# Optimization experiments

Measured on AMD Instinct MI355X. Metric: run time of the kernel, lower is better.

The kernel has to match this reference:

```python
import jax, jax.numpy as jnp
import numpy as np

NL, D, NH, HD, MLP, L = 4, 1280, 16, 80, 5120, 2048
SEG = 512  # patches per packed image


def setup_inputs() -> dict:
    key = jax.random.key(0)
    ks = jax.random.split(key, 16)
    s = 0.02
    # per-segment RoPE frequency table: positions restart at each image boundary
    inv_freq = 1.0 / (10000.0 ** (jnp.arange(0, HD, 2, dtype=jnp.float32) / HD))  # (HD/2,)
    pos = (jnp.arange(L) % SEG).astype(jnp.float32)
    rotary_pos_emb = pos[:, None] * inv_freq[None, :]  # (L, HD/2)
    return {
        "x": jax.random.normal(ks[0], (L, D), jnp.float32),
        "rotary_pos_emb": rotary_pos_emb,
        "cu_seqlens": jnp.array([0, 512, 1024, 1536, 2048], jnp.int32),
        "ln1_g": 1.0 + s * jax.random.normal(ks[1], (NL, D), jnp.float32),
        "ln1_b": s * jax.random.normal(ks[2], (NL, D), jnp.float32),
        "ln2_g": 1.0 + s * jax.random.normal(ks[3], (NL, D), jnp.float32),
        "ln2_b": s * jax.random.normal(ks[4], (NL, D), jnp.float32),
        "qkv_w": s * jax.random.normal(ks[5], (NL, 3 * D, D), jnp.float32),
        "qkv_b": s * jax.random.normal(ks[6], (NL, 3 * D), jnp.float32),
        "proj_w": s * jax.random.normal(ks[7], (NL, D, D), jnp.float32),
        "proj_b": s * jax.random.normal(ks[8], (NL, D), jnp.float32),
        "mlp_w1": s * jax.random.normal(ks[9], (NL, MLP, D), jnp.float32),
        "mlp_b1": s * jax.random.normal(ks[10], (NL, MLP), jnp.float32),
        "mlp_w2": s * jax.random.normal(ks[11], (NL, D, MLP), jnp.float32),
        "mlp_b2": s * jax.random.normal(ks[12], (NL, D), jnp.float32),
    }


def _ln(x, g, b):
    m = jnp.mean(x, axis=-1, keepdims=True)
    v = jnp.mean((x - m) ** 2, axis=-1, keepdims=True)
    return (x - m) * jax.lax.rsqrt(v + 1e-6) * g + b


def _rope(t, cos, sin):
    # t: (L, H, HD); cos/sin: (L, 1, HD)
    half = t.shape[-1] // 2
    rot = jnp.concatenate([-t[..., half:], t[..., :half]], axis=-1)
    return t * cos + rot * sin


def reference(x, rotary_pos_emb, cu_seqlens, ln1_g, ln1_b, ln2_g, ln2_b,
              qkv_w, qkv_b, proj_w, proj_b, mlp_w1, mlp_b1, mlp_w2, mlp_b2):
    Lx = x.shape[0]
    cos = jnp.cos(rotary_pos_emb)
    sin = jnp.sin(rotary_pos_emb)
    cos = jnp.concatenate([cos, cos], axis=-1)[:, None, :]  # (L,1,HD)
    sin = jnp.concatenate([sin, sin], axis=-1)[:, None, :]
    # block-diagonal attention mask from cu_seqlens via segment ids
    seg = jnp.searchsorted(cu_seqlens, jnp.arange(Lx), side="right")  # (L,)
    mask = seg[:, None] == seg[None, :]  # (L,L) bool
    neg = jnp.finfo(jnp.float32).min
    scale = 1.0 / np.sqrt(HD)
    for l in range(qkv_w.shape[0]):
        h = _ln(x, ln1_g[l], ln1_b[l])
        qkv = (h @ qkv_w[l].T + qkv_b[l]).reshape(Lx, 3, NH, HD)
        q, k, v = qkv[:, 0], qkv[:, 1], qkv[:, 2]  # (L,H,HD) each
        q = _rope(q, cos, sin)
        k = _rope(k, cos, sin)
        scores = jnp.einsum("lhd,mhd->hlm", q, k) * scale  # (H,L,L)
        scores = jnp.where(mask[None], scores, neg)
        w = jax.nn.softmax(scores.astype(jnp.float32), axis=-1).astype(x.dtype)
        att = jnp.einsum("hlm,mhd->lhd", w, v).reshape(Lx, NH * HD)
        x = x + att @ proj_w[l].T + proj_b[l]
        h = _ln(x, ln2_g[l], ln2_b[l])
        x = x + jax.nn.gelu(h @ mlp_w1[l].T + mlp_b1[l], approximate=True) @ mlp_w2[l].T + mlp_b2[l]
    return x
```

## Files before the change

kernel.cpp:

```cpp
#include <hip/hip_runtime.h>
#include <cstdint>
#include <cstddef>

typedef unsigned short u16;
typedef __bf16 bf16_t;
typedef bf16_t bf16x8 __attribute__((ext_vector_type(8)));
typedef float f32x4 __attribute__((ext_vector_type(4)));

#define NLAY 4
#define DMODEL 1280
#define NHEAD 16
#define HDIM 80
#define HDP 96
#define MLPD 5120
#define LTOK 2048
#define SEGLEN 512

__device__ __forceinline__ u16 f2bf(float f) {
  union { float f; unsigned u; } x; x.f = f;
  unsigned r = x.u + 0x7fffu + ((x.u >> 16) & 1u);
  return (u16)(r >> 16);
}
__device__ __forceinline__ float bf2f(u16 s) {
  union { unsigned u; float f; } x; x.u = ((unsigned)s) << 16;
  return x.f;
}

#define GLOAD_LDS16(gsrc, ldst) \
  __builtin_amdgcn_global_load_lds((const __attribute__((address_space(1))) void*)(gsrc), \
                                   (__attribute__((address_space(3))) void*)(ldst), 16, 0, 0)

__device__ __forceinline__ void barrier_mem() {
  asm volatile("s_barrier" ::: "memory");
}

#define C0 (3 * DMODEL * DMODEL / 4)
#define C1 (C0 + DMODEL * DMODEL / 4)
#define C2 (C1 + MLPD * DMODEL / 4)
#define C3 (C2 + DMODEL * MLPD / 4)
__global__ __launch_bounds__(256) void cvt4(const float* __restrict__ s_q,
                                            const float* __restrict__ s_p,
                                            const float* __restrict__ s_1,
                                            const float* __restrict__ s_2,
                                            u16* __restrict__ o_q, u16* __restrict__ o_p,
                                            u16* __restrict__ o_1, u16* __restrict__ o_2) {
  int i = blockIdx.x * 256 + threadIdx.x;
  const float* src; u16* dst; int off;
  if (i < C0)      { src = s_q; dst = o_q; off = i; }
  else if (i < C1) { src = s_p; dst = o_p; off = i - C0; }
  else if (i < C2) { src = s_1; dst = o_1; off = i - C1; }
  else if (i < C3) { src = s_2; dst = o_2; off = i - C2; }
  else return;
  const float4 v = reinterpret_cast<const float4*>(src)[off];
  union { u16 s[4]; uint2 u; } o;
  o.s[0] = f2bf(v.x); o.s[1] = f2bf(v.y); o.s[2] = f2bf(v.z); o.s[3] = f2bf(v.w);
  reinterpret_cast<uint2*>(dst)[off] = o.u;
}

__global__ __launch_bounds__(256) void ln_bf16(const float* __restrict__ x,
                                               const float* __restrict__ g,
                                               const float* __restrict__ b,
                                               u16* __restrict__ out) {
  int row = blockIdx.x;
  int t = threadIdx.x;
  const float* xr = x + (size_t)row * DMODEL;
  float v[5]; float s = 0.f, s2 = 0.f;
#pragma unroll
  for (int i = 0; i < 5; i++) { v[i] = xr[t + i * 256]; s += v[i]; s2 += v[i] * v[i]; }
#pragma unroll
  for (int off = 32; off; off >>= 1) { s += __shfl_down(s, off); s2 += __shfl_down(s2, off); }
  __shared__ float ps[4], ps2[4];
  int w = t >> 6;
  if ((t & 63) == 0) { ps[w] = s; ps2[w] = s2; }
  __syncthreads();
  s = ps[0] + ps[1] + ps[2] + ps[3];
  s2 = ps2[0] + ps2[1] + ps2[2] + ps2[3];
  float mean = s * (1.f / DMODEL);
  float var = s2 * (1.f / DMODEL) - mean * mean;
  float inv = rsqrtf(var + 1e-6f);
#pragma unroll
  for (int i = 0; i < 5; i++) {
    int c = t + i * 256;
    out[(size_t)row * DMODEL + c] = f2bf((v[i] - mean) * inv * g[c] + b[c]);
  }
}

template <int EPI>
__global__ __launch_bounds__(512, 4) void gemmhp(const u16* __restrict__ A,
                                                 const u16* __restrict__ B,
                                                 const float* __restrict__ bias,
                                                 u16* __restrict__ Cb,
                                                 int M, int N, int K) {
  __shared__ u16 As[3][128 * 32];
  __shared__ u16 Bs[3][256 * 32];

  int gN = gridDim.x, gM = gridDim.y;
  int flat = blockIdx.x + gN * blockIdx.y;
  int nwg = gN * gM;
  int qc = nwg >> 3, rc = nwg & 7;
  int xcd = flat & 7, pos = flat >> 3;
  int start = (xcd < rc) ? xcd * (qc + 1) : rc * (qc + 1) + (xcd - rc) * qc;
  int swz = start + pos;
  int m0 = (swz % gM) * 128;
  int n0 = (swz / gM) * 256;

  int t = threadIdx.x, lane = t & 63, w = t >> 6;
  int wm = w >> 2, wn = w & 3;
  int r = lane & 15, kq = lane >> 4;
  f32x4 acc[4][4] = {};

  auto stageA = [&](int buf, int k0) {
    int row = t >> 2, s = t & 3;
    int ss = s ^ ((row >> 1) & 3);
    GLOAD_LDS16(A + (size_t)(m0 + row) * K + k0 + ss * 8, &As[buf][t * 8]);
  };
  auto stageB = [&](int buf, int k0) {
#pragma unroll
    for (int i = 0; i < 2; i++) {
      int chunk = i * 512 + t;
      int row = chunk >> 2, s = chunk & 3;
      int ss = s ^ ((row >> 1) & 3);
      GLOAD_LDS16(B + (size_t)(n0 + row) * K + k0 + ss * 8, &Bs[buf][chunk * 8]);
    }
  };

  int NT = K >> 5;
  stageA(0, 0); stageB(0, 0);
  stageA(1, 32); stageB(1, 32);

  int bt = 0;
  for (int kt = 0; kt < NT; kt++) {
    if (kt == NT - 1) asm volatile("s_waitcnt vmcnt(0)" ::: "memory");
    else              asm volatile("s_waitcnt vmcnt(3)" ::: "memory");
    barrier_mem();
    const u16* as = As[bt];
    const u16* bs = Bs[bt];
    int b2 = bt + 2; if (b2 >= 3) b2 -= 3;
    bool st = (kt + 2) < NT;
    int k2 = (kt + 2) << 5;

    bf16x8 af[4], bfv[4];
#pragma unroll
    for (int i = 0; i < 4; i++) {
      int row = wm * 64 + i * 16 + r;
      int ss = kq ^ ((row >> 1) & 3);
      af[i] = *(const bf16x8*)&as[row * 32 + ss * 8];
    }
#pragma unroll
    for (int j = 0; j < 4; j++) {
      int row = wn * 64 + j * 16 + r;
      int ss = kq ^ ((row >> 1) & 3);
      bfv[j] = *(const bf16x8*)&bs[row * 32 + ss * 8];
    }
    if (st) { stageA(b2, k2); stageB(b2, k2); }
    __builtin_amdgcn_s_setprio(1);
#pragma unroll
    for (int i = 0; i < 4; i++)
#pragma unroll
      for (int j = 0; j < 4; j++)
        acc[i][j] = __builtin_amdgcn_mfma_f32_16x16x32_bf16(af[i], bfv[j], acc[i][j], 0, 0, 0);
    __builtin_amdgcn_s_setprio(0);

    bt++; if (bt == 3) bt = 0;
  }

#pragma unroll
  for (int i = 0; i < 4; i++) {
#pragma unroll
    for (int j = 0; j < 4; j++) {
      int col = n0 + wn * 64 + j * 16 + r;
      float bv = bias[col];
#pragma unroll
      for (int reg = 0; reg < 4; reg++) {
        int rowg = m0 + wm * 64 + i * 16 + kq * 4 + reg;
        float val = acc[i][j][reg] + bv;
        if (EPI == 2) {
          float z2 = -1.5957691216057308f * fmaf(0.044715f * val, val * val, val);
          float gg = val / (1.f + __expf(z2));
          Cb[(size_t)rowg * N + col] = f2bf(gg);
        } else {
          Cb[(size_t)rowg * N + col] = f2bf(val);
        }
      }
    }
  }
}

template <int EPI, int BM, int BN>
__global__ __launch_bounds__(256) void gemm_bt(const u16* __restrict__ A,
                                               const u16* __restrict__ B,
                                               const float* __restrict__ bias,
                                               float* __restrict__ Cf,
                                               u16* __restrict__ Cb,
                                               int M, int N, int K) {
  constexpr int MI = BM / 32;
  constexpr int NJ = BN / 32;
  constexpr int ACH = BM * 64 / (256 * 8);
  constexpr int BCH = BN * 64 / (256 * 8);
  __shared__ u16 As[2][BM * 64];
  __shared__ u16 Bs[2][BN * 64];

  int gN = gridDim.x, gM = gridDim.y;
  int flat = blockIdx.x + gN * blockIdx.y;
  int nwg = gN * gM;
  int qc = nwg >> 3, rc = nwg & 7;
  int xcd = flat & 7, pos = flat >> 3;
  int start = (xcd < rc) ? xcd * (qc + 1) : rc * (qc + 1) + (xcd - rc) * qc;
  int swz = start + pos;
  int m0 = (swz % gM) * BM;
  int n0 = (swz / gM) * BN;

  int t = threadIdx.x, lane = t & 63, w = t >> 6;
  int wm = w >> 1, wn = w & 1;
  int r = lane & 15, kq = lane >> 4;
  f32x4 acc[MI][NJ] = {};

  auto stage = [&](int buf, int k0) {
#pragma unroll
    for (int i = 0; i < ACH; i++) {
      int chunk = i * 256 + t;
      int row = chunk >> 3, s = chunk & 7;
      int ss = s ^ (row & 7);
      GLOAD_LDS16(A + (size_t)(m0 + row) * K + k0 + ss * 8, &As[buf][chunk * 8]);
    }
#pragma unroll
    for (int i = 0; i < BCH; i++) {
      int chunk = i * 256 + t;
      int row = chunk >> 3, s = chunk & 7;
      int ss = s ^ (row & 7);
      GLOAD_LDS16(B + (size_t)(n0 + row) * K + k0 + ss * 8, &Bs[buf][chunk * 8]);
    }
  };

  auto compute = [&](int buf) {
#pragma unroll
    for (int kk = 0; kk < 64; kk += 32) {
      int sx8 = (((kk >> 3) + kq) ^ (r & 7)) * 8;
      bf16x8 af[MI], bfr[NJ];
#pragma unroll
      for (int i = 0; i < MI; i++)
        af[i] = *(const bf16x8*)&As[buf][(wm * (BM / 2) + i * 16 + r) * 64 + sx8];
#pragma unroll
      for (int j = 0; j < NJ; j++)
        bfr[j] = *(const bf16x8*)&Bs[buf][(wn * (BN / 2) + j * 16 + r) * 64 + sx8];
#pragma unroll
      for (int i = 0; i < MI; i++)
#pragma unroll
        for (int j = 0; j < NJ; j++)
          acc[i][j] = __builtin_amdgcn_mfma_f32_16x16x32_bf16(af[i], bfr[j], acc[i][j], 0, 0, 0);
    }
  };

  int NT = K >> 6;
  stage(0, 0);
  __syncthreads();
  for (int step = 0; step < NT; step++) {
    int buf = step & 1;
    if (step + 1 < NT) stage(buf ^ 1, (step + 1) * 64);
    compute(buf);
    __syncthreads();
  }

#pragma unroll
  for (int i = 0; i < MI; i++) {
#pragma unroll
    for (int j = 0; j < NJ; j++) {
      int col = n0 + wn * (BN / 2) + j * 16 + r;
      float bv = bias[col];
#pragma unroll
      for (int reg = 0; reg < 4; reg++) {
        int rowg = m0 + wm * (BM / 2) + i * 16 + kq * 4 + reg;
        float val = acc[i][j][reg] + bv;
        if (EPI == 1) {
          Cf[(size_t)rowg * N + col] += val;
        } else {
          Cb[(size_t)rowg * N + col] = f2bf(val);
        }
      }
    }
  }
}

__global__ __launch_bounds__(256) void rope_pack(const u16* __restrict__ qkv,
                                                 const float* __restrict__ rpe,
                                                 u16* __restrict__ qp,
                                                 u16* __restrict__ kp) {
  int l = blockIdx.x;
  int t = threadIdx.x;
  __shared__ float cs[40], sn[40];
  if (t < 40) {
    float a = rpe[l * 40 + t];
    cs[t] = cosf(a);
    sn[t] = sinf(a);
  }
  __syncthreads();
  const u16* row = qkv + (size_t)l * (3 * DMODEL);
  const float scale = 0.11180339887498949f;
#pragma unroll
  for (int i = 0; i < 5; i++) {
    int e = t + i * 256;
    int h = e / HDIM, d = e - h * HDIM;
    int dm = (d < 40) ? d : d - 40;
    float c = cs[dm], s = sn[dm];
    float qv = bf2f(row[h * HDIM + d]);
    float qr = (d < 40) ? -bf2f(row[h * HDIM + d + 40]) : bf2f(row[h * HDIM + d - 40]);
    qp[((size_t)h * LTOK + l) * HDP + d] = f2bf((qv * c + qr * s) * scale);
    float kv = bf2f(row[DMODEL + h * HDIM + d]);
    float kr = (d < 40) ? -bf2f(row[DMODEL + h * HDIM + d + 40]) : bf2f(row[DMODEL + h * HDIM + d - 40]);
    kp[((size_t)h * LTOK + l) * HDP + d] = f2bf(kv * c + kr * s);
  }
  {
    int h = t >> 4, p = t & 15;
    qp[((size_t)h * LTOK + l) * HDP + HDIM + p] = 0;
    kp[((size_t)h * LTOK + l) * HDP + HDIM + p] = 0;
  }
}

__global__ __launch_bounds__(256) void vtrans(const u16* __restrict__ qkv,
                                              u16* __restrict__ vt) {
  int blk = blockIdx.x;
  int h = blk >> 5, lt = blk & 31;
  int t = threadIdx.x;
  __shared__ u16 ld[64][81];
#pragma unroll
  for (int i = 0; i < 20; i++) {
    int idx = t + i * 256;
    int ll = idx / HDIM, d = idx - ll * HDIM;
    ld[ll][d] = qkv[(size_t)(lt * 64 + ll) * (3 * DMODEL) + 2 * DMODEL + h * HDIM + d];
  }
  __syncthreads();
#pragma unroll
  for (int i = 0; i < 20; i++) {
    int idx = t + i * 256;
    int d = idx >> 6, ll = idx & 63;
    vt[((size_t)h * HDIM + d) * LTOK + lt * 64 + ll] = ld[ll][d];
  }
}

__global__ __launch_bounds__(256) void attn(const u16* __restrict__ qp,
                                            const u16* __restrict__ kp,
                                            const u16* __restrict__ vt,
                                            u16* __restrict__ out) {
  int bid = blockIdx.x;
  int h = bid >> 5;
  int seg = (bid >> 3) & 3;
  int qt = bid & 7;
  int t = threadIdx.x, w = t >> 6, lane = t & 63;
  int r = lane & 15, kq = lane >> 4;
  __shared__ u16 P[4][16][512];
  int seg0 = seg * SEGLEN;
  int q0 = seg0 + qt * 64 + w * 16;

  bf16x8 qf[3];
  const u16* qrow = qp + ((size_t)h * LTOK + q0 + r) * HDP;
#pragma unroll
  for (int kk = 0; kk < 3; kk++) qf[kk] = *(const bf16x8*)(qrow + kk * 32 + kq * 8);

  f32x4 sc[32];
#pragma unroll
  for (int j = 0; j < 32; j++) {
    f32x4 a = {0.f, 0.f, 0.f, 0.f};
    const u16* krow = kp + ((size_t)h * LTOK + seg0 + j * 16 + r) * HDP;
#pragma unroll
    for (int kk = 0; kk < 3; kk++) {
      bf16x8 bfr = *(const bf16x8*)(krow + kk * 32 + kq * 8);
      a = __builtin_amdgcn_mfma_f32_16x16x32_bf16(qf[kk], bfr, a, 0, 0, 0);
    }
    sc[j] = a;
  }

#pragma unroll
  for (int rr = 0; rr < 4; rr++) {
    float m = -1e30f;
#pragma unroll
    for (int j = 0; j < 32; j++) m = fmaxf(m, sc[j][rr]);
#pragma unroll
    for (int off = 1; off < 16; off <<= 1) m = fmaxf(m, __shfl_xor(m, off));
    float s = 0.f;
#pragma unroll
    for (int j = 0; j < 32; j++) { float e = __expf(sc[j][rr] - m); sc[j][rr] = e; s += e; }
#pragma unroll
    for (int off = 1; off < 16; off <<= 1) s += __shfl_xor(s, off);
    float inv = 1.f / s;
#pragma unroll
    for (int j = 0; j < 32; j++)
      P[w][kq * 4 + rr][j * 16 + r] = f2bf(sc[j][rr] * inv);
  }
  __syncthreads();

  f32x4 oc[5] = {};
#pragma unroll
  for (int tt = 0; tt < 16; tt++) {
    bf16x8 a = *(const bf16x8*)&P[w][r][tt * 32 + kq * 8];
#pragma unroll
    for (int n = 0; n < 5; n++) {
      const u16* vrow = vt + ((size_t)h * HDIM + n * 16 + r) * LTOK + seg0 + tt * 32 + kq * 8;
      bf16x8 bfr = *(const bf16x8*)vrow;
      oc[n] = __builtin_amdgcn_mfma_f32_16x16x32_bf16(a, bfr, oc[n], 0, 0, 0);
    }
  }
#pragma unroll
  for (int n = 0; n < 5; n++)
#pragma unroll
    for (int reg = 0; reg < 4; reg++) {
      int l = q0 + kq * 4 + reg;
      out[(size_t)l * DMODEL + h * HDIM + n * 16 + r] = f2bf(oc[n][reg]);
    }
}

extern "C" void kernel_launch(void* const* d_in, const int* in_sizes, int n_in,
                              void* d_out, int out_size, void* d_ws, size_t ws_size,
                              hipStream_t stream) {
  (void)in_sizes; (void)n_in; (void)out_size; (void)ws_size;
  const float* x_in   = (const float*)d_in[0];
  const float* rpe    = (const float*)d_in[1];
  const float* ln1_g  = (const float*)d_in[3];
  const float* ln1_b  = (const float*)d_in[4];
  const float* ln2_g  = (const float*)d_in[5];
  const float* ln2_b  = (const float*)d_in[6];
  const float* qkv_w  = (const float*)d_in[7];
  const float* qkv_b  = (const float*)d_in[8];
  const float* proj_w = (const float*)d_in[9];
  const float* proj_b = (const float*)d_in[10];
  const float* mlp_w1 = (const float*)d_in[11];
  const float* mlp_b1 = (const float*)d_in[12];
  const float* mlp_w2 = (const float*)d_in[13];
  const float* mlp_b2 = (const float*)d_in[14];
  float* x = (float*)d_out;

  char* ws = (char*)d_ws;
  size_t off = 0;
  auto alloc = [&](size_t bytes) -> char* {
    char* p = ws + off;
    off = (off + bytes + 255) & ~(size_t)255;
    return p;
  };
  u16* wq  = (u16*)alloc((size_t)3 * DMODEL * DMODEL * 2);
  u16* wp  = (u16*)alloc((size_t)DMODEL * DMODEL * 2);
  u16* w1  = (u16*)alloc((size_t)MLPD * DMODEL * 2);
  u16* w2  = (u16*)alloc((size_t)DMODEL * MLPD * 2);
  u16* hb  = (u16*)alloc((size_t)LTOK * DMODEL * 2);
  u16* qkvb = (u16*)alloc((size_t)LTOK * 3 * DMODEL * 2);
  u16* qp  = (u16*)alloc((size_t)NHEAD * LTOK * HDP * 2);
  u16* kp  = (u16*)alloc((size_t)NHEAD * LTOK * HDP * 2);
  u16* vt  = (u16*)alloc((size_t)NHEAD * HDIM * LTOK * 2);
  u16* att = (u16*)alloc((size_t)LTOK * DMODEL * 2);
  u16* ge  = (u16*)alloc((size_t)LTOK * MLPD * 2);

  hipMemcpyAsync(x, x_in, (size_t)LTOK * DMODEL * sizeof(float),
                 hipMemcpyDeviceToDevice, stream);

  for (int l = 0; l < NLAY; l++) {
    cvt4<<<(C3 + 255) / 256, 256, 0, stream>>>(
        qkv_w + (size_t)l * 3 * DMODEL * DMODEL, proj_w + (size_t)l * DMODEL * DMODEL,
        mlp_w1 + (size_t)l * MLPD * DMODEL, mlp_w2 + (size_t)l * DMODEL * MLPD,
        wq, wp, w1, w2);

    ln_bf16<<<LTOK, 256, 0, stream>>>(x, ln1_g + l * DMODEL, ln1_b + l * DMODEL, hb);
    gemmhp<3><<<dim3(15, 16), 512, 0, stream>>>(
        hb, wq, qkv_b + (size_t)l * 3 * DMODEL, qkvb, LTOK, 3 * DMODEL, DMODEL);
    rope_pack<<<LTOK, 256, 0, stream>>>(qkvb, rpe, qp, kp);
    vtrans<<<NHEAD * 32, 256, 0, stream>>>(qkvb, vt);
    attn<<<NHEAD * 4 * 8, 256, 0, stream>>>(qp, kp, vt, att);
    gemm_bt<1, 64, 64><<<dim3(20, 32), 256, 0, stream>>>(
        att, wp, proj_b + (size_t)l * DMODEL, x, nullptr, LTOK, DMODEL, DMODEL);
    ln_bf16<<<LTOK, 256, 0, stream>>>(x, ln2_g + l * DMODEL, ln2_b + l * DMODEL, hb);
    gemmhp<2><<<dim3(20, 16), 512, 0, stream>>>(
        hb, w1, mlp_b1 + (size_t)l * MLPD, ge, LTOK, MLPD, DMODEL);
    gemm_bt<1, 64, 64><<<dim3(20, 32), 256, 0, stream>>>(
        ge, w2, mlp_b2 + (size_t)l * DMODEL, x, nullptr, LTOK, DMODEL, MLPD);
  }
}
```

Measured before the change: 923.7 us.

## Replace residual GEMMs with 128x128 triple-buffered pipelined kernel

Replaces the 64x64 double-buffered gemm_bt used for the attention projection and MLP down-projection with a new 128x128 tile kernel. It uses BK=32, three LDS buffers with fine-grained vmcnt waits, and raised wave priority around the MFMA block. The goal is more data reuse per tile and better overlap of global loads with compute. The grid shrinks from 640 to 160 workgroups, which may underfill the CUs for the N=1280 GEMMs.

```diff
diff --git a/kernel.cpp b/kernel.cpp
--- a/kernel.cpp
+++ b/kernel.cpp
@@ -186,19 +186,14 @@
   }
 }
 
-template <int EPI, int BM, int BN>
-__global__ __launch_bounds__(256) void gemm_bt(const u16* __restrict__ A,
-                                               const u16* __restrict__ B,
-                                               const float* __restrict__ bias,
-                                               float* __restrict__ Cf,
-                                               u16* __restrict__ Cb,
-                                               int M, int N, int K) {
-  constexpr int MI = BM / 32;
-  constexpr int NJ = BN / 32;
-  constexpr int ACH = BM * 64 / (256 * 8);
-  constexpr int BCH = BN * 64 / (256 * 8);
-  __shared__ u16 As[2][BM * 64];
-  __shared__ u16 Bs[2][BN * 64];
+template <int EPI>
+__global__ __launch_bounds__(256, 3) void gemmdp(const u16* __restrict__ A,
+                                                 const u16* __restrict__ B,
+                                                 const float* __restrict__ bias,
+                                                 float* __restrict__ Cf,
+                                                 int M, int N, int K) {
+  __shared__ u16 As[3][128 * 32];
+  __shared__ u16 Bs[3][128 * 32];
 
   int gN = gridDim.x, gM = gridDim.y;
   int flat = blockIdx.x + gN * blockIdx.y;
@@ -207,75 +202,81 @@
   int xcd = flat & 7, pos = flat >> 3;
   int start = (xcd < rc) ? xcd * (qc + 1) : rc * (qc + 1) + (xcd - rc) * qc;
   int swz = start + pos;
-  int m0 = (swz % gM) * BM;
-  int n0 = (swz / gM) * BN;
+  int m0 = (swz % gM) * 128;
+  int n0 = (swz / gM) * 128;
 
   int t = threadIdx.x, lane = t & 63, w = t >> 6;
   int wm = w >> 1, wn = w & 1;
   int r = lane & 15, kq = lane >> 4;
-  f32x4 acc[MI][NJ] = {};
+  f32x4 acc[4][4] = {};
 
   auto stage = [&](int buf, int k0) {
 #pragma unroll
-    for (int i = 0; i < ACH; i++) {
+    for (int i = 0; i < 2; i++) {
       int chunk = i * 256 + t;
-      int row = chunk >> 3, s = chunk & 7;
-      int ss = s ^ (row & 7);
+      int row = chunk >> 2, s = chunk & 3;
+      int ss = s ^ ((row >> 1) & 3);
       GLOAD_LDS16(A + (size_t)(m0 + row) * K + k0 + ss * 8, &As[buf][chunk * 8]);
     }
 #pragma unroll
-    for (int i = 0; i < BCH; i++) {
+    for (int i = 0; i < 2; i++) {
       int chunk = i * 256 + t;
-      int row = chunk >> 3, s = chunk & 7;
-      int ss = s ^ (row & 7);
+      int row = chunk >> 2, s = chunk & 3;
+      int ss = s ^ ((row >> 1) & 3);
       GLOAD_LDS16(B + (size_t)(n0 + row) * K + k0 + ss * 8, &Bs[buf][chunk * 8]);
     }
   };
 
-  auto compute = [&](int buf) {
-#pragma unroll
-    for (int kk = 0; kk < 64; kk += 32) {
-      int sx8 = (((kk >> 3) + kq) ^ (r & 7)) * 8;
-      bf16x8 af[MI], bfr[NJ];
-#pragma unroll
-      for (int i = 0; i < MI; i++)
-        af[i] = *(const bf16x8*)&As[buf][(wm * (BM / 2) + i * 16 + r) * 64 + sx8];
-#pragma unroll
-      for (int j = 0; j < NJ; j++)
-        bfr[j] = *(const bf16x8*)&Bs[buf][(wn * (BN / 2) + j * 16 + r) * 64 + sx8];
-#pragma unroll
-      for (int i = 0; i < MI; i++)
-#pragma unroll
-        for (int j = 0; j < NJ; j++)
-          acc[i][j] = __builtin_amdgcn_mfma_f32_16x16x32_bf16(af[i], bfr[j], acc[i][j], 0, 0, 0);
-    }
-  };
-
-  int NT = K >> 6;
+  int NT = K >> 5;
   stage(0, 0);
-  __syncthreads();
-  for (int step = 0; step < NT; step++) {
-    int buf = step & 1;
-    if (step + 1 < NT) stage(buf ^ 1, (step + 1) * 64);
-    compute(buf);
-    __syncthreads();
-  }
-
-#pragma unroll
-  for (int i = 0; i < MI; i++) {
-#pragma unroll
-    for (int j = 0; j < NJ; j++) {
-      int col = n0 + wn * (BN / 2) + j * 16 + r;
+  stage(1, 32);
+
+  int bt = 0;
+  for (int kt = 0; kt < NT; kt++) {
+    if (kt == NT - 1) asm volatile("s_waitcnt vmcnt(0)" ::: "memory");
+    else              asm volatile("s_waitcnt vmcnt(4)" ::: "memory");
+    barrier_mem();
+    const u16* as = As[bt];
+    const u16* bs = Bs[bt];
+    int b2 = bt + 2; if (b2 >= 3) b2 -= 3;
+    bool st = (kt + 2) < NT;
+    int k2 = (kt + 2) << 5;
+
+    bf16x8 af[4], bfv[4];
+#pragma unroll
+    for (int i = 0; i < 4; i++) {
+      int row = wm * 64 + i * 16 + r;
+      int ss = kq ^ ((row >> 1) & 3);
+      af[i] = *(const bf16x8*)&as[row * 32 + ss * 8];
+    }
+#pragma unroll
+    for (int j = 0; j < 4; j++) {
+      int row = wn * 64 + j * 16 + r;
+      int ss = kq ^ ((row >> 1) & 3);
+      bfv[j] = *(const bf16x8*)&bs[row * 32 + ss * 8];
+    }
+    if (st) stage(b2, k2);
+    __builtin_amdgcn_s_setprio(1);
+#pragma unroll
+    for (int i = 0; i < 4; i++)
+#pragma unroll
+      for (int j = 0; j < 4; j++)
+        acc[i][j] = __builtin_amdgcn_mfma_f32_16x16x32_bf16(af[i], bfv[j], acc[i][j], 0, 0, 0);
+    __builtin_amdgcn_s_setprio(0);
+
+    bt++; if (bt == 3) bt = 0;
+  }
+
+#pragma unroll
+  for (int i = 0; i < 4; i++) {
+#pragma unroll
+    for (int j = 0; j < 4; j++) {
+      int col = n0 + wn * 64 + j * 16 + r;
       float bv = bias[col];
 #pragma unroll
       for (int reg = 0; reg < 4; reg++) {
-        int rowg = m0 + wm * (BM / 2) + i * 16 + kq * 4 + reg;
-        float val = acc[i][j][reg] + bv;
-        if (EPI == 1) {
-          Cf[(size_t)rowg * N + col] += val;
-        } else {
-          Cb[(size_t)rowg * N + col] = f2bf(val);
-        }
+        int rowg = m0 + wm * 64 + i * 16 + kq * 4 + reg;
+        Cf[(size_t)rowg * N + col] += acc[i][j][reg] + bv;
       }
     }
   }
@@ -462,12 +463,12 @@
     rope_pack<<<LTOK, 256, 0, stream>>>(qkvb, rpe, qp, kp);
     vtrans<<<NHEAD * 32, 256, 0, stream>>>(qkvb, vt);
     attn<<<NHEAD * 4 * 8, 256, 0, stream>>>(qp, kp, vt, att);
-    gemm_bt<1, 64, 64><<<dim3(20, 32), 256, 0, stream>>>(
-        att, wp, proj_b + (size_t)l * DMODEL, x, nullptr, LTOK, DMODEL, DMODEL);
+    gemmdp<1><<<dim3(10, 16), 256, 0, stream>>>(
+        att, wp, proj_b + (size_t)l * DMODEL, x, LTOK, DMODEL, DMODEL);
     ln_bf16<<<LTOK, 256, 0, stream>>>(x, ln2_g + l * DMODEL, ln2_b + l * DMODEL, hb);
     gemmhp<2><<<dim3(20, 16), 512, 0, stream>>>(
         hb, w1, mlp_b1 + (size_t)l * MLPD, ge, LTOK, MLPD, DMODEL);
-    gemm_bt<1, 64, 64><<<dim3(20, 32), 256, 0, stream>>>(
-        ge, w2, mlp_b2 + (size_t)l * DMODEL, x, nullptr, LTOK, DMODEL, MLPD);
-  }
-}
+    gemmdp<1><<<dim3(10, 16), 256, 0, stream>>>(
+        ge, w2, mlp_b2 + (size_t)l * DMODEL, x, LTOK, DMODEL, MLPD);
+  }
+}
```

Measured after the change: 1.078 ms. 16.7% more time.

## Split-K the MLP down-projection with 128x128 tiles and separate reduction

Applied to the files above, without the earlier changes.

Replaces the 64x64-tile down-projection GEMM (K=5120) with a 4-way split-K kernel. It uses 128x128 tiles and a triple-buffered LDS pipeline, and writes fp32 partials into dead workspace buffers starting at hb. A separate reduce kernel then sums the partials, adds the bias and accumulates into the residual x. The aim is more data reuse per tile while keeping enough workgroups to fill the GPU. In exchange, the partials cost extra memory traffic and a second kernel launch per layer.

```diff
diff --git a/kernel.cpp b/kernel.cpp
--- a/kernel.cpp
+++ b/kernel.cpp
@@ -186,6 +186,120 @@
   }
 }
 
+__global__ __launch_bounds__(256, 3) void gemmsk(const u16* __restrict__ A,
+                                                 const u16* __restrict__ B,
+                                                 float* __restrict__ P,
+                                                 int M, int N, int K, int KC) {
+  __shared__ u16 As[3][128 * 32];
+  __shared__ u16 Bs[3][128 * 32];
+
+  int gN = gridDim.x, gM = gridDim.y;
+  int flat = blockIdx.x + gN * blockIdx.y;
+  int nwg = gN * gM;
+  int qc = nwg >> 3, rc = nwg & 7;
+  int xcd = flat & 7, pos = flat >> 3;
+  int start = (xcd < rc) ? xcd * (qc + 1) : rc * (qc + 1) + (xcd - rc) * qc;
+  int swz = start + pos;
+  int m0 = (swz % gM) * 128;
+  int n0 = (swz / gM) * 128;
+  int kbase = blockIdx.z * KC;
+  float* Pz = P + (size_t)blockIdx.z * M * N;
+
+  int t = threadIdx.x, lane = t & 63, w = t >> 6;
+  int wm = w >> 1, wn = w & 1;
+  int r = lane & 15, kq = lane >> 4;
+  f32x4 acc[4][4] = {};
+
+  auto stage = [&](int buf, int k0) {
+#pragma unroll
+    for (int i = 0; i < 2; i++) {
+      int chunk = i * 256 + t;
+      int row = chunk >> 2, s = chunk & 3;
+      int ss = s ^ ((row >> 1) & 3);
+      GLOAD_LDS16(A + (size_t)(m0 + row) * K + k0 + ss * 8, &As[buf][chunk * 8]);
+    }
+#pragma unroll
+    for (int i = 0; i < 2; i++) {
+      int chunk = i * 256 + t;
+      int row = chunk >> 2, s = chunk & 3;
+      int ss = s ^ ((row >> 1) & 3);
+      GLOAD_LDS16(B + (size_t)(n0 + row) * K + k0 + ss * 8, &Bs[buf][chunk * 8]);
+    }
+  };
+
+  int NT = KC >> 5;
+  stage(0, kbase);
+  stage(1, kbase + 32);
+
+  int bt = 0;
+  for (int kt = 0; kt < NT; kt++) {
+    if (kt == NT - 1) asm volatile("s_waitcnt vmcnt(0)" ::: "memory");
+    else              asm volatile("s_waitcnt vmcnt(4)" ::: "memory");
+    barrier_mem();
+    const u16* as = As[bt];
+    const u16* bs = Bs[bt];
+    int b2 = bt + 2; if (b2 >= 3) b2 -= 3;
+    bool st = (kt + 2) < NT;
+    int k2 = kbase + ((kt + 2) << 5);
+
+    bf16x8 af[4], bfv[4];
+#pragma unroll
+    for (int i = 0; i < 4; i++) {
+      int row = wm * 64 + i * 16 + r;
+      int ss = kq ^ ((row >> 1) & 3);
+      af[i] = *(const bf16x8*)&as[row * 32 + ss * 8];
+    }
+#pragma unroll
+    for (int j = 0; j < 4; j++) {
+      int row = wn * 64 + j * 16 + r;
+      int ss = kq ^ ((row >> 1) & 3);
+      bfv[j] = *(const bf16x8*)&bs[row * 32 + ss * 8];
+    }
+    if (st) stage(b2, k2);
+    __builtin_amdgcn_s_setprio(1);
+#pragma unroll
+    for (int i = 0; i < 4; i++)
+#pragma unroll
+      for (int j = 0; j < 4; j++)
+        acc[i][j] = __builtin_amdgcn_mfma_f32_16x16x32_bf16(af[i], bfv[j], acc[i][j], 0, 0, 0);
+    __builtin_amdgcn_s_setprio(0);
+
+    bt++; if (bt == 3) bt = 0;
+  }
+
+#pragma unroll
+  for (int i = 0; i < 4; i++) {
+#pragma unroll
+    for (int j = 0; j < 4; j++) {
+      int col = n0 + wn * 64 + j * 16 + r;
+#pragma unroll
+      for (int reg = 0; reg < 4; reg++) {
+        int rowg = m0 + wm * 64 + i * 16 + kq * 4 + reg;
+        Pz[(size_t)rowg * N + col] = acc[i][j][reg];
+      }
+    }
+  }
+}
+
+#define N4TOT (LTOK * DMODEL / 4)
+__global__ __launch_bounds__(256) void reduce4(const float4* __restrict__ P,
+                                               const float* __restrict__ bias,
+                                               float4* __restrict__ x) {
+  int i = blockIdx.x * 256 + threadIdx.x;
+  if (i >= N4TOT) return;
+  float4 a = P[i];
+  float4 b = P[i + N4TOT];
+  float4 c = P[i + 2 * N4TOT];
+  float4 d = P[i + 3 * N4TOT];
+  float4 bv = reinterpret_cast<const float4*>(bias)[i % (DMODEL / 4)];
+  float4 xv = x[i];
+  xv.x += a.x + b.x + c.x + d.x + bv.x;
+  xv.y += a.y + b.y + c.y + d.y + bv.y;
+  xv.z += a.z + b.z + c.z + d.z + bv.z;
+  xv.w += a.w + b.w + c.w + d.w + bv.w;
+  x[i] = xv;
+}
+
 template <int EPI, int BM, int BN>
 __global__ __launch_bounds__(256) void gemm_bt(const u16* __restrict__ A,
                                                const u16* __restrict__ B,
@@ -446,6 +560,7 @@
   u16* vt  = (u16*)alloc((size_t)NHEAD * HDIM * LTOK * 2);
   u16* att = (u16*)alloc((size_t)LTOK * DMODEL * 2);
   u16* ge  = (u16*)alloc((size_t)LTOK * MLPD * 2);
+  float* pk = (float*)hb;
 
   hipMemcpyAsync(x, x_in, (size_t)LTOK * DMODEL * sizeof(float),
                  hipMemcpyDeviceToDevice, stream);
@@ -467,7 +582,9 @@
     ln_bf16<<<LTOK, 256, 0, stream>>>(x, ln2_g + l * DMODEL, ln2_b + l * DMODEL, hb);
     gemmhp<2><<<dim3(20, 16), 512, 0, stream>>>(
         hb, w1, mlp_b1 + (size_t)l * MLPD, ge, LTOK, MLPD, DMODEL);
-    gemm_bt<1, 64, 64><<<dim3(20, 32), 256, 0, stream>>>(
-        ge, w2, mlp_b2 + (size_t)l * DMODEL, x, nullptr, LTOK, DMODEL, MLPD);
-  }
-}
+    gemmsk<<<dim3(10, 16, 4), 256, 0, stream>>>(
+        ge, w2, pk, LTOK, DMODEL, MLPD, MLPD / 4);
+    reduce4<<<(N4TOT + 255) / 256, 256, 0, stream>>>(
+        (const float4*)pk, mlp_b2 + (size_t)l * DMODEL, (float4*)x);
+  }
+}
```

Result: no change. 928.5 us (+0.5%).
